# Kernel optimization log

Measured on AMD Instinct MI355X. Metric: run time of the kernel, lower is better.

The kernel has to match this reference:

```python
import jax, jax.numpy as jnp
import numpy as np

B, T, IN, H = 4096, 19, 17, 1024


def setup_inputs() -> dict:
    key = jax.random.key(0)
    ks = jax.random.split(key, 7)
    s = 0.05
    return {
        "x": jax.random.normal(ks[0], (B, T, IN), dtype=jnp.float32),
        "W_ih": jax.random.normal(ks[1], (4 * H, IN), dtype=jnp.float32) * s,
        "W_hh": jax.random.normal(ks[2], (4 * H, H), dtype=jnp.float32) * s,
        "b_ih": jax.random.normal(ks[3], (4 * H,), dtype=jnp.float32) * s,
        "b_hh": jax.random.normal(ks[4], (4 * H,), dtype=jnp.float32) * s,
        "W_lin": jax.random.normal(ks[5], (IN, H), dtype=jnp.float32) * s,
        "b_lin": jax.random.normal(ks[6], (IN,), dtype=jnp.float32) * s,
    }


def reference(x, W_ih, W_hh, b_ih, b_hh, W_lin, b_lin):
    # x: [B, T, IN]; PyTorch LSTMCell gate order is i, f, g, o.
    batch = x.shape[0]
    hid = W_hh.shape[1]
    h0 = jnp.zeros((batch, hid), dtype=x.dtype)
    c0 = jnp.zeros((batch, hid), dtype=x.dtype)

    def step(carry, xt):
        h, c = carry
        gates = xt @ W_ih.T + b_ih + h @ W_hh.T + b_hh  # [B, 4H]
        i, f, g, o = jnp.split(gates, 4, axis=-1)
        i = jax.nn.sigmoid(i)
        f = jax.nn.sigmoid(f)
        g = jnp.tanh(g)
        o = jax.nn.sigmoid(o)
        c_new = f * c + i * g
        h_new = o * jnp.tanh(c_new)
        out = h_new @ W_lin.T + b_lin  # [B, IN]
        return (h_new, c_new), out

    (h_fin, c_fin), outs = jax.lax.scan(step, (h0, c0), jnp.swapaxes(x, 0, 1))
    output = jnp.swapaxes(outs, 0, 1)  # [B, T, IN]
    return output, h_fin, c_fin
```

## Files before the change

### kernel.cpp

```cpp
#include <hip/hip_runtime.h>
#include <hip/hip_bf16.h>

typedef unsigned short u16;
typedef __attribute__((ext_vector_type(8))) __bf16 bf16x8;
typedef __attribute__((ext_vector_type(8))) short short8;
typedef __attribute__((ext_vector_type(4))) float f32x4;

#define BB 4096
#define TT 19
#define INP 17
#define HH 1024
#define NE 4128
#define NT_PROJ 15

#define ABASE(b) ((b) * 16384)
#define BBASE(b) (32768 + (b) * 16384)
#define PBASE(b) (65536 + (b) * 2048)
#define LDS_BYTES 139264

#define FENCE asm volatile("" ::: "memory")

__device__ __forceinline__ u16 f2bfu(float f) {
    __hip_bfloat16 b = __float2bfloat16(f);
    return __builtin_bit_cast(unsigned short, b);
}
__device__ __forceinline__ float fast_sigmoid(float x) {
    return 1.f / (1.f + __expf(-x));
}
__device__ __forceinline__ float fast_tanh(float x) {
    float e = __expf(2.f * x);
    return (e - 1.f) / (e + 1.f);
}
__device__ __forceinline__ bf16x8 ldfrag(const u16* p) {
    return __builtin_bit_cast(bf16x8, *(const short8*)p);
}
__device__ __forceinline__ int cBase(int row) {
    return row < 128 ? 16384 + row * 128 : 49152 + (row - 128) * 128;
}
__device__ __forceinline__ void cp16(const u16* l, const void* g) {
    __builtin_amdgcn_global_load_lds(
        (const __attribute__((address_space(1))) unsigned int*)g,
        (__attribute__((address_space(3))) unsigned int*)l, 16, 0, 0);
}

__global__ void prep_wperm(const float* __restrict__ Whh, const float* __restrict__ Wlin,
                           u16* __restrict__ wperm) {
    size_t idx = ((size_t)blockIdx.x * 256 + threadIdx.x) * 8;
    int R = (int)(idx >> 10);
    int k = (int)(idx & 1023);
    const float* src = nullptr;
    if (R < 4096) {
        int nt = R >> 8, r = R & 255;
        int qn = r >> 6, nf = (r >> 4) & 3, cj = r & 15;
        int hcol = nt * 64 + qn * 16 + cj;
        src = Whh + ((size_t)(nf * HH + hcol)) * HH + k;
    } else if (R - 4096 < INP) {
        src = Wlin + (size_t)(R - 4096) * HH + k;
    }
#pragma unroll
    for (int e = 0; e < 8; ++e) wperm[idx + e] = src ? f2bfu(src[e]) : (u16)0;
}

__global__ void prep_wx64(const float* __restrict__ Wih, u16* __restrict__ wx64) {
    int idx = blockIdx.x * 256 + threadIdx.x;
    int R = idx >> 6, k = idx & 63;
    u16 v = 0;
    if (R < 4096 && k < INP) {
        int nt = R >> 8, r = R & 255;
        int qn = r >> 6, nf = (r >> 4) & 3, cj = r & 15;
        int hcol = nt * 64 + qn * 16 + cj;
        v = f2bfu(Wih[(size_t)(nf * HH + hcol) * INP + k]);
    }
    wx64[idx] = v;
}

__global__ void prep_bias(const float* __restrict__ bih, const float* __restrict__ bhh,
                          float* __restrict__ bias) {
    int idx = blockIdx.x * 256 + threadIdx.x;
    bias[idx] = bih[idx] + bhh[idx];
}

__global__ void prep_x64(const float* __restrict__ x, u16* __restrict__ xpad) {
    int idx = blockIdx.x * 256 + threadIdx.x;
    int c = idx & 63;
    int rb = idx >> 6;
    int t = rb >> 12;
    int b = rb & 4095;
    xpad[idx] = (c < INP) ? f2bfu(x[((size_t)b * TT + t) * INP + c]) : (u16)0;
}

__global__ __launch_bounds__(512, 2) void lstm_step(
    const u16* __restrict__ h_in, u16* __restrict__ h_out,
    float* __restrict__ c_buf, const u16* __restrict__ wperm,
    const u16* __restrict__ wx64, const float* __restrict__ bias,
    const u16* __restrict__ xpad64, const float* __restrict__ blin,
    float* __restrict__ outp, float* __restrict__ h_fin,
    int t, int is_last, int tail)
{
    extern __shared__ u16 lds[];

    const int tid = threadIdx.x;
    const int lane = tid & 63;
    const int wv = tid >> 6;
    const int qr = wv >> 2, qn = wv & 3;
    const int r16 = lane & 15, s4 = lane >> 4;

    int mt, nt;
    if (tail) { mt = blockIdx.x; nt = NT_PROJ; }
    else {
        const int xcd = blockIdx.x & 7, local = blockIdx.x >> 3;
        mt = (xcd >> 2) * 8 + (local & 7);
        nt = (xcd & 3) * 4 + (local >> 3);
    }
    const int m0 = mt * 256;
    const size_t R0 = (size_t)nt * 256;
    const bool my_proj = (nt == NT_PROJ) && (qn < 2);
    const int NK = (tail || t > 0) ? 17 : 1;

    int srow[4], sgc[4];
#pragma unroll
    for (int i = 0; i < 4; ++i) {
        int d = tid + i * 512;
        srow[i] = d >> 3;
        sgc[i] = (d & 7) ^ (srow[i] & 7);
    }
    const u16* hA[4];
    const u16* wB[4];
#pragma unroll
    for (int i = 0; i < 4; ++i) {
        hA[i] = h_in + (size_t)(m0 + srow[i]) * HH + sgc[i] * 8;
        wB[i] = wperm + (R0 + srow[i]) * HH + sgc[i] * 8;
    }
    const int prow = (tid >> 3) & 31;
    const int pgc = (tid & 7) ^ (prow & 7);
    const u16* wP = wperm + (size_t)(4096 + prow) * HH + pgc * 8;

    int aoff[8], boff[4], poff;
#pragma unroll
    for (int mf = 0; mf < 8; ++mf) {
        int r = qr * 128 + mf * 16 + r16;
        aoff[mf] = r * 64 + ((s4 ^ (r & 7)) * 8);
    }
#pragma unroll
    for (int nf = 0; nf < 4; ++nf) {
        int r = qn * 64 + nf * 16 + r16;
        boff[nf] = r * 64 + ((s4 ^ (r & 7)) * 8);
    }
    {
        int r = qn * 16 + r16;
        poff = r * 64 + ((s4 ^ (r & 7)) * 8);
    }

    f32x4 acc[8][4];
    const int n = nt * 64 + qn * 16 + r16;
    if (!tail) {
#pragma unroll
        for (int nf = 0; nf < 4; ++nf) {
            float bv = bias[nf * HH + n];
#pragma unroll
            for (int mf = 0; mf < 8; ++mf) acc[mf][nf] = (f32x4){bv, bv, bv, bv};
        }
    }
    f32x4 pacc[8];
    const int p = qn * 16 + r16;
    if (my_proj) {
        float pv = (p < INP) ? blin[p] : 0.f;
#pragma unroll
        for (int mf = 0; mf < 8; ++mf) pacc[mf] = (f32x4){pv, pv, pv, pv};
    }

    const u16* xA = xpad64 + ((size_t)t * BB + m0) * 64;
#pragma unroll
    for (int i = 0; i < 4; ++i)
        cp16(&lds[ABASE(0) + (tid + i * 512) * 8], xA + (size_t)srow[i] * 64 + sgc[i] * 8);
#pragma unroll
    for (int i = 0; i < 4; ++i)
        cp16(&lds[BBASE(0) + (tid + i * 512) * 8], wx64 + (R0 + srow[i]) * 64 + sgc[i] * 8);
    if (wv < 4) cp16(&lds[PBASE(0) + tid * 8], wP);

    for (int j = 0; j < NK; ++j) {
        const int cb = j & 1, nb = cb ^ 1;
        if (j < NK - 1) {
            const int ko = j * 64;
#pragma unroll
            for (int i = 0; i < 4; ++i)
                cp16(&lds[ABASE(nb) + (tid + i * 512) * 8], hA[i] + ko);
#pragma unroll
            for (int i = 0; i < 4; ++i)
                cp16(&lds[BBASE(nb) + (tid + i * 512) * 8], wB[i] + ko);
            if (wv < 4) {
                cp16(&lds[PBASE(nb) + tid * 8], wP + ko);
                asm volatile("s_waitcnt vmcnt(9)" ::: "memory");
            } else {
                asm volatile("s_waitcnt vmcnt(8)" ::: "memory");
            }
        } else if (!tail) {
#pragma unroll
            for (int i = 0; i < 8; ++i) {
                const int s = tid + i * 512;
                const int crow = s >> 4, cch = s & 15;
                const u16* dst = (i < 4) ? &lds[16384 + s * 8] : &lds[32768 + s * 8];
                cp16(dst, c_buf + (size_t)(m0 + crow) * HH + nt * 64 + cch * 4);
            }
            asm volatile("s_waitcnt vmcnt(8)" ::: "memory");
        } else {
            asm volatile("s_waitcnt vmcnt(0)" ::: "memory");
        }
        __builtin_amdgcn_s_barrier();
        FENCE;

        const int cbA = ABASE(cb), cbB = BBASE(cb), cbP = PBASE(cb);
        const bool do_p = my_proj && (j > 0);
        __builtin_amdgcn_s_setprio(1);
#pragma unroll
        for (int kk = 0; kk < 2; ++kk) {
            const int kx = kk * 32;
            bf16x8 b[4];
            if (!tail) {
#pragma unroll
                for (int nf = 0; nf < 4; ++nf)
                    b[nf] = ldfrag(&lds[cbB + (boff[nf] ^ kx)]);
            }
            bf16x8 pb;
            if (do_p) pb = ldfrag(&lds[cbP + (poff ^ kx)]);
#pragma unroll
            for (int h2 = 0; h2 < 2; ++h2) {
                bf16x8 a[4];
#pragma unroll
                for (int i = 0; i < 4; ++i)
                    a[i] = ldfrag(&lds[cbA + (aoff[h2 * 4 + i] ^ kx)]);
                if (!tail) {
#pragma unroll
                    for (int nf = 0; nf < 4; ++nf)
#pragma unroll
                        for (int i = 0; i < 4; ++i)
                            acc[h2 * 4 + i][nf] = __builtin_amdgcn_mfma_f32_16x16x32_bf16(
                                a[i], b[nf], acc[h2 * 4 + i][nf], 0, 0, 0);
                }
                if (do_p) {
#pragma unroll
                    for (int i = 0; i < 4; ++i)
                        pacc[h2 * 4 + i] = __builtin_amdgcn_mfma_f32_16x16x32_bf16(
                            a[i], pb, pacc[h2 * 4 + i], 0, 0, 0);
                }
            }
        }
        __builtin_amdgcn_s_setprio(0);
        FENCE;
        __builtin_amdgcn_s_barrier();
        FENCE;
    }

    if (!tail) {
        asm volatile("s_waitcnt vmcnt(0)" ::: "memory");
        __syncthreads();
        const int cl = qn * 16 + r16;
#pragma unroll
        for (int mf = 0; mf < 8; ++mf)
#pragma unroll
            for (int j = 0; j < 4; ++j) {
                int rl = qr * 128 + mf * 16 + s4 * 4 + j;
                float iv = fast_sigmoid(acc[mf][0][j]);
                float fv = fast_sigmoid(acc[mf][1][j]);
                float gv = fast_tanh(acc[mf][2][j]);
                float ov = fast_sigmoid(acc[mf][3][j]);
                float* crow = (float*)&lds[cBase(rl)];
                float cold = crow[cl];
                float cnew = fv * cold + iv * gv;
                float hnew = ov * fast_tanh(cnew);
                crow[cl] = cnew;
                lds[rl * 64 + cl] = f2bfu(hnew);
                if (is_last)
                    __builtin_nontemporal_store(
                        hnew, &h_fin[(size_t)(m0 + rl) * HH + n]);
            }
        __syncthreads();
#pragma unroll 4
        for (int r = 0; r < 32; ++r) {
            const int rl = wv * 32 + r;
            const size_t gi = (size_t)(m0 + rl) * HH + nt * 64 + lane;
            c_buf[gi] = ((float*)&lds[cBase(rl)])[lane];
            h_out[gi] = lds[rl * 64 + lane];
        }
    }
    if (my_proj && t > 0 && p < INP) {
#pragma unroll
        for (int mf = 0; mf < 8; ++mf)
#pragma unroll
            for (int j = 0; j < 4; ++j) {
                int row = m0 + qr * 128 + mf * 16 + s4 * 4 + j;
                __builtin_nontemporal_store(
                    pacc[mf][j], &outp[((size_t)row * TT + (t - 1)) * INP + p]);
            }
    }
}

extern "C" void kernel_launch(void* const* d_in, const int* in_sizes, int n_in,
                              void* d_out, int out_size, void* d_ws, size_t ws_size,
                              hipStream_t stream)
{
    const float* x    = (const float*)d_in[0];
    const float* Wih  = (const float*)d_in[1];
    const float* Whh  = (const float*)d_in[2];
    const float* bih  = (const float*)d_in[3];
    const float* bhh  = (const float*)d_in[4];
    const float* Wlin = (const float*)d_in[5];
    const float* blin = (const float*)d_in[6];
    float* out = (float*)d_out;

    char* ws = (char*)d_ws;
    u16* hb0     = (u16*)(ws);
    u16* hb1     = (u16*)(ws +  8388608);
    u16* xpad64  = (u16*)(ws + 16777216);
    u16* wperm   = (u16*)(ws + 27262976);
    u16* wx64    = (u16*)(ws + 35717120);
    float* bias  = (float*)(ws + 36245504);

    float* h_fin = out + (size_t)BB * TT * INP;
    float* c_buf = h_fin + (size_t)BB * HH;

    hipFuncSetAttribute((const void*)lstm_step,
                        hipFuncAttributeMaxDynamicSharedMemorySize, LDS_BYTES);

    hipMemsetAsync(c_buf, 0, (size_t)BB * HH * sizeof(float), stream);
    hipMemsetAsync((char*)xpad64 + (size_t)19 * BB * 64 * 2, 0, BB * 64 * 2, stream);

    prep_wperm<<<2064, 256, 0, stream>>>(Whh, Wlin, wperm);
    prep_wx64<<<1032, 256, 0, stream>>>(Wih, wx64);
    prep_bias<<<16, 256, 0, stream>>>(bih, bhh, bias);
    prep_x64<<<19456, 256, 0, stream>>>(x, xpad64);

    for (int t = 0; t < TT; ++t) {
        const u16* hin = (t & 1) ? hb1 : hb0;
        u16* hout = (t & 1) ? hb0 : hb1;
        lstm_step<<<256, 512, LDS_BYTES, stream>>>(
            hin, hout, c_buf, wperm, wx64, bias, xpad64, blin, out,
            h_fin, t, (t == TT - 1) ? 1 : 0, 0);
    }
    lstm_step<<<16, 512, LDS_BYTES, stream>>>(
        hb1, hb0, c_buf, wperm, wx64, bias, xpad64, blin, out,
        h_fin, TT, 0, 1);
}
```

Baseline: 1.016 ms.

## Split K-tile into half-tiles and interleave global loads with MFMA phases

Restructures the LSTM gate GEMM main loop into four phases per 64-wide K step. Each phase issues part of the next tile's global-to-LDS copies while computing MFMAs on the current tile. LDS layout changes to two 32-wide K halves with a new 4-way XOR swizzle. The goal is finer overlap between memory traffic and matrix math. The cost is more barriers per iteration and tighter hand-tuned vmcnt waits, which could stall or introduce hazards.

```diff
diff --git a/kernel.cpp b/kernel.cpp
--- a/kernel.cpp
+++ b/kernel.cpp
@@ -13,9 +13,9 @@
 #define NE 4128
 #define NT_PROJ 15
 
-#define ABASE(b) ((b) * 16384)
-#define BBASE(b) (32768 + (b) * 16384)
-#define PBASE(b) (65536 + (b) * 2048)
+#define AH(b,k) ((b) * 16384 + (k) * 8192)
+#define BH(b,k) (32768 + (b) * 16384 + (k) * 8192)
+#define PH(b,k) (65536 + (b) * 2048 + (k) * 1024)
 #define LDS_BYTES 139264
 
 #define FENCE asm volatile("" ::: "memory")
@@ -34,6 +34,7 @@
 __device__ __forceinline__ bf16x8 ldfrag(const u16* p) {
     return __builtin_bit_cast(bf16x8, *(const short8*)p);
 }
+__device__ __forceinline__ int fsw(int r) { return (r ^ (r >> 2)) & 3; }
 __device__ __forceinline__ int cBase(int row) {
     return row < 128 ? 16384 + row * 128 : 49152 + (row - 128) * 128;
 }
@@ -117,38 +118,35 @@
     const bool my_proj = (nt == NT_PROJ) && (qn < 2);
     const int NK = (tail || t > 0) ? 17 : 1;
 
-    int srow[4], sgc[4];
-#pragma unroll
-    for (int i = 0; i < 4; ++i) {
-        int d = tid + i * 512;
-        srow[i] = d >> 3;
-        sgc[i] = (d & 7) ^ (srow[i] & 7);
-    }
-    const u16* hA[4];
-    const u16* wB[4];
-#pragma unroll
-    for (int i = 0; i < 4; ++i) {
-        hA[i] = h_in + (size_t)(m0 + srow[i]) * HH + sgc[i] * 8;
-        wB[i] = wperm + (R0 + srow[i]) * HH + sgc[i] * 8;
-    }
-    const int prow = (tid >> 3) & 31;
-    const int pgc = (tid & 7) ^ (prow & 7);
-    const u16* wP = wperm + (size_t)(4096 + prow) * HH + pgc * 8;
+    const int sr0 = tid >> 2, sr1 = (tid + 512) >> 2;
+    const int gc0 = (((tid & 3) ^ fsw(sr0)) & 3) * 8;
+    const int gc1 = (((tid & 3) ^ fsw(sr1)) & 3) * 8;
+    const u16* srcA0 = h_in + (size_t)(m0 + sr0) * HH + gc0;
+    const u16* srcA1 = h_in + (size_t)(m0 + sr1) * HH + gc1;
+    const u16* srcB0 = wperm + (R0 + sr0) * HH + gc0;
+    const u16* srcB1 = wperm + (R0 + sr1) * HH + gc1;
+    const int psr = (tid >> 2) & 31;
+    const int pgc = (((tid & 3) ^ fsw(psr)) & 3) * 8;
+    const u16* srcP = wperm + (size_t)(4096 + psr) * HH + pgc;
+    const u16* xA0 = xpad64 + ((size_t)t * BB + m0 + sr0) * 64 + gc0;
+    const u16* xA1 = xpad64 + ((size_t)t * BB + m0 + sr1) * 64 + gc1;
+    const u16* xB0 = wx64 + (R0 + sr0) * 64 + gc0;
+    const u16* xB1 = wx64 + (R0 + sr1) * 64 + gc1;
 
     int aoff[8], boff[4], poff;
 #pragma unroll
     for (int mf = 0; mf < 8; ++mf) {
         int r = qr * 128 + mf * 16 + r16;
-        aoff[mf] = r * 64 + ((s4 ^ (r & 7)) * 8);
+        aoff[mf] = r * 32 + ((s4 ^ fsw(r)) & 3) * 8;
     }
 #pragma unroll
     for (int nf = 0; nf < 4; ++nf) {
         int r = qn * 64 + nf * 16 + r16;
-        boff[nf] = r * 64 + ((s4 ^ (r & 7)) * 8);
+        boff[nf] = r * 32 + ((s4 ^ fsw(r)) & 3) * 8;
     }
     {
         int r = qn * 16 + r16;
-        poff = r * 64 + ((s4 ^ (r & 7)) * 8);
+        poff = r * 32 + ((s4 ^ fsw(r)) & 3) * 8;
     }
 
     f32x4 acc[8][4];
@@ -169,86 +167,103 @@
         for (int mf = 0; mf < 8; ++mf) pacc[mf] = (f32x4){pv, pv, pv, pv};
     }
 
-    const u16* xA = xpad64 + ((size_t)t * BB + m0) * 64;
-#pragma unroll
-    for (int i = 0; i < 4; ++i)
-        cp16(&lds[ABASE(0) + (tid + i * 512) * 8], xA + (size_t)srow[i] * 64 + sgc[i] * 8);
-#pragma unroll
-    for (int i = 0; i < 4; ++i)
-        cp16(&lds[BBASE(0) + (tid + i * 512) * 8], wx64 + (R0 + srow[i]) * 64 + sgc[i] * 8);
-    if (wv < 4) cp16(&lds[PBASE(0) + tid * 8], wP);
-
+#pragma unroll
+    for (int k = 0; k < 2; ++k) {
+        cp16(&lds[AH(0, k) + tid * 8],         xA0 + k * 32);
+        cp16(&lds[AH(0, k) + (tid + 512) * 8], xA1 + k * 32);
+        cp16(&lds[BH(0, k) + tid * 8],         xB0 + k * 32);
+        cp16(&lds[BH(0, k) + (tid + 512) * 8], xB1 + k * 32);
+    }
+    asm volatile("s_waitcnt vmcnt(0)" ::: "memory");
+    FENCE;
+    __builtin_amdgcn_s_barrier();
+    FENCE;
+
+#pragma unroll 1
     for (int j = 0; j < NK; ++j) {
         const int cb = j & 1, nb = cb ^ 1;
-        if (j < NK - 1) {
-            const int ko = j * 64;
+        const bool lastj = (j == NK - 1);
+        const int ko = j * 64;
+        const bool dp = my_proj && (j > 0);
+        bf16x8 bfr[4];
+        bf16x8 pbf;
+#pragma unroll
+        for (int ph = 0; ph < 4; ++ph) {
+            const int kk = ph >> 1, mg = ph & 1;
+            bf16x8 afr[4];
+            if (mg == 0) {
+                if (!tail) {
+#pragma unroll
+                    for (int nf = 0; nf < 4; ++nf)
+                        bfr[nf] = ldfrag(&lds[BH(cb, kk) + boff[nf]]);
+                }
+                if (dp) pbf = ldfrag(&lds[PH(cb, kk) + poff]);
+            }
 #pragma unroll
             for (int i = 0; i < 4; ++i)
-                cp16(&lds[ABASE(nb) + (tid + i * 512) * 8], hA[i] + ko);
-#pragma unroll
-            for (int i = 0; i < 4; ++i)
-                cp16(&lds[BBASE(nb) + (tid + i * 512) * 8], wB[i] + ko);
-            if (wv < 4) {
-                cp16(&lds[PBASE(nb) + tid * 8], wP + ko);
-                asm volatile("s_waitcnt vmcnt(9)" ::: "memory");
-            } else {
-                asm volatile("s_waitcnt vmcnt(8)" ::: "memory");
-            }
-        } else if (!tail) {
-#pragma unroll
-            for (int i = 0; i < 8; ++i) {
-                const int s = tid + i * 512;
-                const int crow = s >> 4, cch = s & 15;
-                const u16* dst = (i < 4) ? &lds[16384 + s * 8] : &lds[32768 + s * 8];
-                cp16(dst, c_buf + (size_t)(m0 + crow) * HH + nt * 64 + cch * 4);
-            }
-            asm volatile("s_waitcnt vmcnt(8)" ::: "memory");
-        } else {
-            asm volatile("s_waitcnt vmcnt(0)" ::: "memory");
+                afr[i] = ldfrag(&lds[AH(cb, kk) + aoff[mg * 4 + i]]);
+
+            if (!lastj) {
+                if (ph == 0) {
+                    cp16(&lds[AH(nb, 0) + tid * 8],         srcA0 + ko);
+                    cp16(&lds[AH(nb, 0) + (tid + 512) * 8], srcA1 + ko);
+                } else if (ph == 1) {
+                    cp16(&lds[BH(nb, 0) + tid * 8],         srcB0 + ko);
+                    cp16(&lds[BH(nb, 0) + (tid + 512) * 8], srcB1 + ko);
+                    if (wv < 2) cp16(&lds[PH(nb, 0) + tid * 8], srcP + ko);
+                } else if (ph == 2) {
+                    cp16(&lds[AH(nb, 1) + tid * 8],         srcA0 + ko + 32);
+                    cp16(&lds[AH(nb, 1) + (tid + 512) * 8], srcA1 + ko + 32);
+                } else {
+                    cp16(&lds[BH(nb, 1) + tid * 8],         srcB0 + ko + 32);
+                    cp16(&lds[BH(nb, 1) + (tid + 512) * 8], srcB1 + ko + 32);
+                    if (wv < 2) cp16(&lds[PH(nb, 1) + tid * 8], srcP + ko + 32);
+                }
+            } else if (!tail) {
+                const int i0 = 2 * ph, i1 = 2 * ph + 1;
+                const int s0 = tid + i0 * 512, s1 = tid + i1 * 512;
+                cp16((i0 < 4) ? &lds[16384 + s0 * 8] : &lds[32768 + s0 * 8],
+                     c_buf + (size_t)(m0 + (s0 >> 4)) * HH + nt * 64 + (s0 & 15) * 4);
+                cp16((i1 < 4) ? &lds[16384 + s1 * 8] : &lds[32768 + s1 * 8],
+                     c_buf + (size_t)(m0 + (s1 >> 4)) * HH + nt * 64 + (s1 & 15) * 4);
+            }
+            FENCE;
+            __builtin_amdgcn_s_barrier();
+            asm volatile("s_waitcnt lgkmcnt(0)" ::: "memory");
+            __builtin_amdgcn_sched_barrier(0);
+            __builtin_amdgcn_s_setprio(1);
+            if (!tail) {
+#pragma unroll
+                for (int nf = 0; nf < 4; ++nf)
+#pragma unroll
+                    for (int i = 0; i < 4; ++i)
+                        acc[mg * 4 + i][nf] = __builtin_amdgcn_mfma_f32_16x16x32_bf16(
+                            afr[i], bfr[nf], acc[mg * 4 + i][nf], 0, 0, 0);
+            }
+            if (dp) {
+#pragma unroll
+                for (int i = 0; i < 4; ++i)
+                    pacc[mg * 4 + i] = __builtin_amdgcn_mfma_f32_16x16x32_bf16(
+                        afr[i], pbf, pacc[mg * 4 + i], 0, 0, 0);
+            }
+            __builtin_amdgcn_s_setprio(0);
+            FENCE;
+            if (ph == 1) {
+                if (lastj) {
+                    if (!tail) asm volatile("s_waitcnt vmcnt(4)" ::: "memory");
+                    else       asm volatile("s_waitcnt vmcnt(0)" ::: "memory");
+                } else if (wv < 2) {
+                    asm volatile("s_waitcnt vmcnt(5)" ::: "memory");
+                } else {
+                    asm volatile("s_waitcnt vmcnt(4)" ::: "memory");
+                }
+            } else if (ph == 3 && !lastj) {
+                if (wv < 2) asm volatile("s_waitcnt vmcnt(5)" ::: "memory");
+                else        asm volatile("s_waitcnt vmcnt(4)" ::: "memory");
+            }
+            __builtin_amdgcn_s_barrier();
+            FENCE;
         }
-        __builtin_amdgcn_s_barrier();
-        FENCE;
-
-        const int cbA = ABASE(cb), cbB = BBASE(cb), cbP = PBASE(cb);
-        const bool do_p = my_proj && (j > 0);
-        __builtin_amdgcn_s_setprio(1);
-#pragma unroll
-        for (int kk = 0; kk < 2; ++kk) {
-            const int kx = kk * 32;
-            bf16x8 b[4];
-            if (!tail) {
-#pragma unroll
-                for (int nf = 0; nf < 4; ++nf)
-                    b[nf] = ldfrag(&lds[cbB + (boff[nf] ^ kx)]);
-            }
-            bf16x8 pb;
-            if (do_p) pb = ldfrag(&lds[cbP + (poff ^ kx)]);
-#pragma unroll
-            for (int h2 = 0; h2 < 2; ++h2) {
-                bf16x8 a[4];
-#pragma unroll
-                for (int i = 0; i < 4; ++i)
-                    a[i] = ldfrag(&lds[cbA + (aoff[h2 * 4 + i] ^ kx)]);
-                if (!tail) {
-#pragma unroll
-                    for (int nf = 0; nf < 4; ++nf)
-#pragma unroll
-                        for (int i = 0; i < 4; ++i)
-                            acc[h2 * 4 + i][nf] = __builtin_amdgcn_mfma_f32_16x16x32_bf16(
-                                a[i], b[nf], acc[h2 * 4 + i][nf], 0, 0, 0);
-                }
-                if (do_p) {
-#pragma unroll
-                    for (int i = 0; i < 4; ++i)
-                        pacc[h2 * 4 + i] = __builtin_amdgcn_mfma_f32_16x16x32_bf16(
-                            a[i], pb, pacc[h2 * 4 + i], 0, 0, 0);
-                }
-            }
-        }
-        __builtin_amdgcn_s_setprio(0);
-        FENCE;
-        __builtin_amdgcn_s_barrier();
-        FENCE;
     }
 
     if (!tail) {
```

After: 1.091 ms. +7.4%, slower.
